# Kernel optimization log

Hardware: AMD Instinct MI355X
Metric: run time of the kernel (lower is better)

Reference implementation:

```python
import jax, jax.numpy as jnp
import numpy as np

B, N, D = 4, 2048, 256
H = 8
HD = D // H
FF = 1024
EPS = 1e-5


def layer_norm(x, g, b):
    mu = jnp.mean(x, axis=-1, keepdims=True)
    var = jnp.mean((x - mu) ** 2, axis=-1, keepdims=True)
    return (x - mu) * jax.lax.rsqrt(var + EPS) * g + b


def setup_inputs() -> dict:
    key = jax.random.key(0)
    ks = jax.random.split(key, 12)
    s = 0.02
    return {
        "tokens": jax.random.normal(ks[0], (B, N, D), dtype=jnp.float32),
        "key_padding_mask": jnp.zeros((B, N), dtype=bool),
        "ln1_g": jnp.ones((D,), jnp.float32),
        "ln1_b": jnp.zeros((D,), jnp.float32),
        "wq": jax.random.normal(ks[1], (D, D), jnp.float32) * s,
        "bq": jnp.zeros((D,), jnp.float32),
        "wk": jax.random.normal(ks[2], (D, D), jnp.float32) * s,
        "bk": jnp.zeros((D,), jnp.float32),
        "wv": jax.random.normal(ks[3], (D, D), jnp.float32) * s,
        "bv": jnp.zeros((D,), jnp.float32),
        "wo": jax.random.normal(ks[4], (D, D), jnp.float32) * s,
        "bo": jnp.zeros((D,), jnp.float32),
        "ln2_g": jnp.ones((D,), jnp.float32),
        "ln2_b": jnp.zeros((D,), jnp.float32),
        "w1": jax.random.normal(ks[5], (D, FF), jnp.float32) * s,
        "b1": jnp.zeros((FF,), jnp.float32),
        "w2": jax.random.normal(ks[6], (FF, D), jnp.float32) * s,
        "b2": jnp.zeros((D,), jnp.float32),
    }


def reference(tokens, key_padding_mask, ln1_g, ln1_b, wq, bq, wk, bk, wv, bv,
              wo, bo, ln2_g, ln2_b, w1, b1, w2, b2):
    x = tokens
    # --- self-attention sublayer (pre-LN) ---
    xn = layer_norm(x, ln1_g, ln1_b)
    q = (xn @ wq + bq).reshape(B, N, H, HD).transpose(0, 2, 1, 3)  # [B,H,N,HD]
    k = (xn @ wk + bk).reshape(B, N, H, HD).transpose(0, 2, 1, 3)
    v = (xn @ wv + bv).reshape(B, N, H, HD).transpose(0, 2, 1, 3)
    scores = jnp.einsum('bhqd,bhkd->bhqk', q, k) / np.sqrt(HD).astype(np.float32)
    scores = jnp.where(key_padding_mask[:, None, None, :], -jnp.inf, scores)
    probs = jax.nn.softmax(scores, axis=-1)
    attn = jnp.einsum('bhqk,bhkd->bhqd', probs, v)
    attn = attn.transpose(0, 2, 1, 3).reshape(B, N, D)
    x = x + (attn @ wo + bo)
    # --- feed-forward sublayer (pre-LN) ---
    xn2 = layer_norm(x, ln2_g, ln2_b)
    h = jax.nn.gelu(xn2 @ w1 + b1, approximate=False)  # torch GELU is exact erf
    x = x + (h @ w2 + b2)
    return x
```

## Files before the change

kernel.cpp:

```cpp
#include <hip/hip_runtime.h>
#include <cmath>

typedef __attribute__((ext_vector_type(8))) __bf16 bf16x8;
typedef __attribute__((ext_vector_type(4))) __bf16 bf16x4;
typedef __attribute__((ext_vector_type(4))) float  f32x4;

constexpr int NB   = 4;
constexpr int SEQ  = 2048;
constexpr int DM   = 256;
constexpr int NH   = 8;
constexpr int DH   = 32;
constexpr int DFF  = 1024;
constexpr int MTOK = NB * SEQ;

__global__ __launch_bounds__(256) void ln_kernel(const float* __restrict__ x,
                                                 const float* __restrict__ g,
                                                 const float* __restrict__ b,
                                                 __bf16* __restrict__ out) {
  int wave = threadIdx.x >> 6, lane = threadIdx.x & 63;
  int row = blockIdx.x * 4 + wave;
  const float* xr = x + (size_t)row * DM;
  f32x4 v = *(const f32x4*)(xr + lane * 4);
  float s  = v[0] + v[1] + v[2] + v[3];
  float sq = v[0]*v[0] + v[1]*v[1] + v[2]*v[2] + v[3]*v[3];
  #pragma unroll
  for (int off = 1; off < 64; off <<= 1) {
    s  += __shfl_xor(s, off);
    sq += __shfl_xor(sq, off);
  }
  float mu  = s * (1.0f / DM);
  float var = sq * (1.0f / DM) - mu * mu;
  float rs  = rsqrtf(var + 1e-5f);
  f32x4 gv = *(const f32x4*)(g + lane * 4);
  f32x4 bv = *(const f32x4*)(b + lane * 4);
  bf16x4 o;
  #pragma unroll
  for (int i = 0; i < 4; ++i) o[i] = (__bf16)((v[i] - mu) * rs * gv[i] + bv[i]);
  *(bf16x4*)(out + (size_t)row * DM + lane * 4) = o;
}

__global__ __launch_bounds__(256) void prep_kernel(
    const float* __restrict__ wq, const float* __restrict__ wk, const float* __restrict__ wv,
    const float* __restrict__ wo, const float* __restrict__ w1, const float* __restrict__ w2,
    const unsigned char* __restrict__ mask, const float* __restrict__ tokens,
    const float* __restrict__ ln1g, const float* __restrict__ ln1b,
    __bf16* __restrict__ wqkvT, __bf16* __restrict__ woT,
    __bf16* __restrict__ w1T, __bf16* __restrict__ w2T,
    float* __restrict__ madd_g, __bf16* __restrict__ xn1) {
  __shared__ float tile[32][33];
  int z = blockIdx.z;
  int tid = threadIdx.x;
  if (z == 6) {
    if (blockIdx.x) return;
    int idx = blockIdx.y * 256 + tid;
    madd_g[idx] = mask[idx] ? -__builtin_inff() : 0.0f;
    return;
  }
  if (z >= 7) {
    int lb = blockIdx.y * 32 + blockIdx.x;
    int row = (z - 7) * 4096 + lb * 4 + (tid >> 6);
    int lane = tid & 63;
    const float* xr = tokens + (size_t)row * DM;
    f32x4 v = *(const f32x4*)(xr + lane * 4);
    float s  = v[0] + v[1] + v[2] + v[3];
    float sq = v[0]*v[0] + v[1]*v[1] + v[2]*v[2] + v[3]*v[3];
    #pragma unroll
    for (int off = 1; off < 64; off <<= 1) {
      s  += __shfl_xor(s, off);
      sq += __shfl_xor(sq, off);
    }
    float mu  = s * (1.0f / DM);
    float var = sq * (1.0f / DM) - mu * mu;
    float rs  = rsqrtf(var + 1e-5f);
    f32x4 gv = *(const f32x4*)(ln1g + lane * 4);
    f32x4 bv = *(const f32x4*)(ln1b + lane * 4);
    bf16x4 o;
    #pragma unroll
    for (int i = 0; i < 4; ++i) o[i] = (__bf16)((v[i] - mu) * rs * gv[i] + bv[i]);
    *(bf16x4*)(xn1 + (size_t)row * DM + lane * 4) = o;
    return;
  }
  const float* W; __bf16* Wt; int K, N;
  if      (z == 0) { W = wq; Wt = wqkvT;          K = 256;  N = 256;  }
  else if (z == 1) { W = wk; Wt = wqkvT + 65536;  K = 256;  N = 256;  }
  else if (z == 2) { W = wv; Wt = wqkvT + 131072; K = 256;  N = 256;  }
  else if (z == 3) { W = wo; Wt = woT;            K = 256;  N = 256;  }
  else if (z == 4) { W = w1; Wt = w1T;            K = 256;  N = 1024; }
  else             { W = w2; Wt = w2T;            K = 1024; N = 256;  }
  int n0 = blockIdx.x * 32, k0 = blockIdx.y * 32;
  if (n0 >= N || k0 >= K) return;
  {
    int kl = tid >> 3, n4 = (tid & 7) * 4;
    f32x4 v = *(const f32x4*)(W + (size_t)(k0 + kl) * N + n0 + n4);
    tile[kl][n4 + 0] = v[0]; tile[kl][n4 + 1] = v[1];
    tile[kl][n4 + 2] = v[2]; tile[kl][n4 + 3] = v[3];
  }
  __syncthreads();
  {
    int nl = tid >> 3, k4 = (tid & 7) * 4;
    bf16x4 o;
    #pragma unroll
    for (int i = 0; i < 4; ++i) o[i] = (__bf16)tile[k4 + i][nl];
    *(bf16x4*)(Wt + (size_t)(n0 + nl) * K + k0 + k4) = o;
  }
}

__global__ __launch_bounds__(256) void transpose_v(const __bf16* __restrict__ V,
                                                   __bf16* __restrict__ Vt) {
  __shared__ __bf16 tile[64][40];
  int tok0 = blockIdx.x * 64;
  int bh = blockIdx.y;
  int tid = threadIdx.x;
  {
    int tl = tid >> 2, h8 = (tid & 3) * 8;
    *(bf16x8*)&tile[tl][h8] = *(const bf16x8*)(V + ((size_t)bh * SEQ + tok0 + tl) * DH + h8);
  }
  __syncthreads();
  {
    int hl = tid >> 3, t8 = (tid & 7) * 8;
    bf16x8 o;
    #pragma unroll
    for (int i = 0; i < 8; ++i) o[i] = tile[t8 + i][hl];
    *(bf16x8*)(Vt + ((size_t)bh * DH + hl) * SEQ + tok0 + t8) = o;
  }
}

template<int BM, int BN, int EP>
__global__ __launch_bounds__(256) void gemm_bt(
    const __bf16* __restrict__ A, const __bf16* __restrict__ Bt,
    int M, int N, int K,
    const float* __restrict__ bias,
    const float* __restrict__ bq, const float* __restrict__ bk, const float* __restrict__ bv,
    const float* __restrict__ resid, float* __restrict__ outf,
    __bf16* __restrict__ outb,
    __bf16* __restrict__ outq, __bf16* __restrict__ outk, __bf16* __restrict__ outv) {
  constexpr int MT = BM / 32, NT = BN / 32;
  constexpr int AP = BM / 32, BP = BN / 32;
  __shared__ __bf16 As[BM * 64];
  __shared__ __bf16 Bs[BN * 64];
  int tid = threadIdx.x;
  int wave = tid >> 6, lane = tid & 63;
  int wm = wave >> 1, wn = wave & 1;
  int quad = lane >> 4, l16 = lane & 15;
  int m0 = blockIdx.x * BM, n0 = blockIdx.y * BN;
  int lrow = lane >> 3;
  int lcg  = ((lane & 7) ^ lrow) * 8;

  f32x4 acc[MT][NT];
  #pragma unroll
  for (int mt = 0; mt < MT; ++mt)
    #pragma unroll
    for (int nt = 0; nt < NT; ++nt)
      #pragma unroll
      for (int r = 0; r < 4; ++r) acc[mt][nt][r] = 0.0f;

  bf16x8 ap[AP], bp[BP];
  #pragma unroll
  for (int i = 0; i < AP; ++i) {
    int rbase = wave * (BM / 4) + i * 8;
    ap[i] = *(const bf16x8*)(A + (size_t)(m0 + rbase + lrow) * K + lcg);
  }
  #pragma unroll
  for (int i = 0; i < BP; ++i) {
    int rbase = wave * (BN / 4) + i * 8;
    bp[i] = *(const bf16x8*)(Bt + (size_t)(n0 + rbase + lrow) * K + lcg);
  }
  #pragma unroll
  for (int i = 0; i < AP; ++i) {
    int rbase = wave * (BM / 4) + i * 8;
    *(bf16x8*)&As[rbase * 64 + lane * 8] = ap[i];
  }
  #pragma unroll
  for (int i = 0; i < BP; ++i) {
    int rbase = wave * (BN / 4) + i * 8;
    *(bf16x8*)&Bs[rbase * 64 + lane * 8] = bp[i];
  }
  __syncthreads();

  for (int kt = 0; kt < K; kt += 64) {
    bool more = (kt + 64) < K;
    if (more) {
      #pragma unroll
      for (int i = 0; i < AP; ++i) {
        int rbase = wave * (BM / 4) + i * 8;
        ap[i] = *(const bf16x8*)(A + (size_t)(m0 + rbase + lrow) * K + kt + 64 + lcg);
      }
      #pragma unroll
      for (int i = 0; i < BP; ++i) {
        int rbase = wave * (BN / 4) + i * 8;
        bp[i] = *(const bf16x8*)(Bt + (size_t)(n0 + rbase + lrow) * K + kt + 64 + lcg);
      }
    }
    #pragma unroll
    for (int ks = 0; ks < 2; ++ks) {
      bf16x8 af[MT], bfr[NT];
      #pragma unroll
      for (int mt = 0; mt < MT; ++mt) {
        int row = wm * (BM / 2) + mt * 16 + l16;
        af[mt] = *(const bf16x8*)&As[row * 64 + (((ks * 4 + quad) ^ (l16 & 7)) * 8)];
      }
      #pragma unroll
      for (int nt = 0; nt < NT; ++nt) {
        int row = wn * (BN / 2) + nt * 16 + l16;
        bfr[nt] = *(const bf16x8*)&Bs[row * 64 + (((ks * 4 + quad) ^ (l16 & 7)) * 8)];
      }
      #pragma unroll
      for (int mt = 0; mt < MT; ++mt)
        #pragma unroll
        for (int nt = 0; nt < NT; ++nt)
          acc[mt][nt] = __builtin_amdgcn_mfma_f32_16x16x32_bf16(af[mt], bfr[nt], acc[mt][nt], 0, 0, 0);
    }
    if (more) {
      __syncthreads();
      #pragma unroll
      for (int i = 0; i < AP; ++i) {
        int rbase = wave * (BM / 4) + i * 8;
        *(bf16x8*)&As[rbase * 64 + lane * 8] = ap[i];
      }
      #pragma unroll
      for (int i = 0; i < BP; ++i) {
        int rbase = wave * (BN / 4) + i * 8;
        *(bf16x8*)&Bs[rbase * 64 + lane * 8] = bp[i];
      }
      __syncthreads();
    }
  }

  #pragma unroll
  for (int mt = 0; mt < MT; ++mt)
  #pragma unroll
  for (int nt = 0; nt < NT; ++nt)
  #pragma unroll
  for (int r = 0; r < 4; ++r) {
    int gm = m0 + wm * (BM / 2) + mt * 16 + quad * 4 + r;
    int gn = n0 + wn * (BN / 2) + nt * 16 + l16;
    float v = acc[mt][nt][r];
    if constexpr (EP == 0) {
      int which = gn >> 8, nn = gn & 255;
      const float* bp2 = which == 0 ? bq : (which == 1 ? bk : bv);
      v += bp2[nn];
      int h = nn >> 5, hd = nn & 31;
      int bb = gm >> 11, tok = gm & 2047;
      __bf16* dst = which == 0 ? outq : (which == 1 ? outk : outv);
      dst[(((size_t)(bb * NH + h)) * SEQ + tok) * DH + hd] = (__bf16)v;
    } else if constexpr (EP == 1) {
      v += bias[gn] + resid[(size_t)gm * N + gn];
      outf[(size_t)gm * N + gn] = v;
    } else {
      v += bias[gn];
      outb[(size_t)gm * N + gn] = (__bf16)(0.5f * v * (1.0f + erff(v * 0.70710678118654752f)));
    }
  }
}

__global__ __launch_bounds__(64) void attn_kernel(
    const __bf16* __restrict__ Q, const __bf16* __restrict__ K,
    const __bf16* __restrict__ Vt, const float* __restrict__ madd_g,
    __bf16* __restrict__ out) {
  constexpr float C2 = 0.2550350030061664f;
  __shared__ __bf16 Ps[2][16][72];
  int bh = blockIdx.x;
  int qw = blockIdx.y * 32;
  int b  = bh >> 3, h = bh & 7;
  int lane = threadIdx.x & 63;
  int quad = lane >> 4, l16 = lane & 15;
  const __bf16* Qb = Q  + (size_t)bh * SEQ * DH;
  const __bf16* Kb = K  + (size_t)bh * SEQ * DH;
  const __bf16* Vb = Vt + (size_t)bh * DH * SEQ;
  const float* maddb = madd_g + b * SEQ;

  bf16x8 qf[2];
  #pragma unroll
  for (int qg = 0; qg < 2; ++qg)
    qf[qg] = *(const bf16x8*)(Qb + (size_t)(qw + qg * 16 + l16) * DH + quad * 8);

  bf16x8 ones;
  #pragma unroll
  for (int i = 0; i < 8; ++i) ones[i] = (__bf16)1.0f;

  f32x4 o[2][2], ol[2];
  #pragma unroll
  for (int qg = 0; qg < 2; ++qg) {
    #pragma unroll
    for (int nt = 0; nt < 2; ++nt)
      #pragma unroll
      for (int r = 0; r < 4; ++r) o[qg][nt][r] = 0.0f;
    #pragma unroll
    for (int r = 0; r < 4; ++r) ol[qg][r] = 0.0f;
  }

  for (int kt = 0; kt < SEQ / 64; ++kt) {
    int k0 = kt * 64;

    f32x4 s[2][4];
    f32x4 zf; zf[0] = zf[1] = zf[2] = zf[3] = 0.0f;
    #pragma unroll
    for (int mt = 0; mt < 4; ++mt) {
      bf16x8 kf = *(const bf16x8*)(Kb + (size_t)(k0 + mt * 16 + l16) * DH + quad * 8);
      s[0][mt] = __builtin_amdgcn_mfma_f32_16x16x32_bf16(kf, qf[0], zf, 0, 0, 0);
      s[1][mt] = __builtin_amdgcn_mfma_f32_16x16x32_bf16(kf, qf[1], zf, 0, 0, 0);
    }

    #pragma unroll
    for (int mt = 0; mt < 4; ++mt) {
      f32x4 md = *(const f32x4*)(maddb + k0 + mt * 16 + quad * 4);
      #pragma unroll
      for (int qg = 0; qg < 2; ++qg) {
        bf16x4 pv;
        #pragma unroll
        for (int r = 0; r < 4; ++r)
          pv[r] = (__bf16)__builtin_amdgcn_exp2f(fmaf(s[qg][mt][r], C2, md[r]));
        *(bf16x4*)&Ps[qg][l16][mt * 16 + quad * 4] = pv;
      }
    }

    #pragma unroll
    for (int ks = 0; ks < 2; ++ks) {
      bf16x8 vf[2];
      #pragma unroll
      for (int nt = 0; nt < 2; ++nt)
        vf[nt] = *(const bf16x8*)(Vb + (size_t)(nt * 16 + l16) * SEQ + k0 + ks * 32 + quad * 8);
      #pragma unroll
      for (int qg = 0; qg < 2; ++qg) {
        bf16x8 pf = *(const bf16x8*)&Ps[qg][l16][ks * 32 + quad * 8];
        #pragma unroll
        for (int nt = 0; nt < 2; ++nt)
          o[qg][nt] = __builtin_amdgcn_mfma_f32_16x16x32_bf16(pf, vf[nt], o[qg][nt], 0, 0, 0);
        ol[qg] = __builtin_amdgcn_mfma_f32_16x16x32_bf16(pf, ones, ol[qg], 0, 0, 0);
      }
    }
  }

  #pragma unroll
  for (int qg = 0; qg < 2; ++qg) {
    f32x4 inv;
    #pragma unroll
    for (int r = 0; r < 4; ++r) inv[r] = 1.0f / ol[qg][r];
    #pragma unroll
    for (int nt = 0; nt < 2; ++nt)
      #pragma unroll
      for (int r = 0; r < 4; ++r) {
        int q   = qw + qg * 16 + quad * 4 + r;
        int col = h * DH + nt * 16 + l16;
        out[((size_t)(b * SEQ + q)) * DM + col] = (__bf16)(o[qg][nt][r] * inv[r]);
      }
  }
}

extern "C" void kernel_launch(void* const* d_in, const int* in_sizes, int n_in,
                              void* d_out, int out_size, void* d_ws, size_t ws_size,
                              hipStream_t stream) {
  const float* tokens = (const float*)d_in[0];
  const unsigned char* mask = (const unsigned char*)d_in[1];
  const float* ln1g = (const float*)d_in[2];
  const float* ln1b = (const float*)d_in[3];
  const float* wq = (const float*)d_in[4];
  const float* bq = (const float*)d_in[5];
  const float* wk = (const float*)d_in[6];
  const float* bk = (const float*)d_in[7];
  const float* wv = (const float*)d_in[8];
  const float* bv = (const float*)d_in[9];
  const float* wo = (const float*)d_in[10];
  const float* bo = (const float*)d_in[11];
  const float* ln2g = (const float*)d_in[12];
  const float* ln2b = (const float*)d_in[13];
  const float* w1 = (const float*)d_in[14];
  const float* b1 = (const float*)d_in[15];
  const float* w2 = (const float*)d_in[16];
  const float* b2 = (const float*)d_in[17];
  float* out = (float*)d_out;
  char* ws = (char*)d_ws;

  __bf16* wqkvT = (__bf16*)(ws + 0);
  __bf16* woT   = (__bf16*)(ws + 393216);
  __bf16* w1T   = (__bf16*)(ws + 524288);
  __bf16* w2T   = (__bf16*)(ws + 1048576);
  __bf16* xn1   = (__bf16*)(ws + 1572864);
  __bf16* qb    = (__bf16*)(ws + 5767168);
  __bf16* kb    = (__bf16*)(ws + 9961472);
  __bf16* vb    = (__bf16*)(ws + 14155776);
  __bf16* vt    = (__bf16*)(ws + 18350080);
  __bf16* attn  = (__bf16*)(ws + 22544384);
  float*  x1    = (float*)(ws + 26738688);
  __bf16* xn2   = (__bf16*)(ws + 35127296);
  __bf16* hbuf  = (__bf16*)(ws + 39321600);
  float*  madd  = (float*)(ws + 56098816);

  prep_kernel<<<dim3(32, 32, 9), 256, 0, stream>>>(
      wq, wk, wv, wo, w1, w2, mask, tokens, ln1g, ln1b,
      wqkvT, woT, w1T, w2T, madd, xn1);

  gemm_bt<128, 128, 0><<<dim3(64, 6), 256, 0, stream>>>(
      xn1, wqkvT, MTOK, 768, 256, nullptr, bq, bk, bv,
      nullptr, nullptr, nullptr, qb, kb, vb);

  transpose_v<<<dim3(SEQ / 64, 32), 256, 0, stream>>>(vb, vt);

  attn_kernel<<<dim3(32, SEQ / 32), 64, 0, stream>>>(qb, kb, vt, madd, attn);

  gemm_bt<64, 64, 1><<<dim3(128, 4), 256, 0, stream>>>(
      attn, woT, MTOK, 256, 256, bo, nullptr, nullptr, nullptr,
      tokens, x1, nullptr, nullptr, nullptr, nullptr);

  ln_kernel<<<MTOK / 4, 256, 0, stream>>>(x1, ln2g, ln2b, xn2);

  gemm_bt<128, 128, 2><<<dim3(64, 8), 256, 0, stream>>>(
      xn2, w1T, MTOK, DFF, 256, b1, nullptr, nullptr, nullptr,
      nullptr, nullptr, hbuf, nullptr, nullptr, nullptr);

  gemm_bt<64, 64, 1><<<dim3(128, 4), 256, 0, stream>>>(
      hbuf, w2T, MTOK, 256, DFF, b2, nullptr, nullptr, nullptr,
      x1, out, nullptr, nullptr, nullptr, nullptr);
}
```

Baseline: 207.4 us.

## Compact prep grid, fuse V transpose into QKV epilogue, pipeline attention, fast GELU

The prep kernel now runs on a flat 1D grid with no empty blocks, where the old 3D grid of 32x32x9 launched many blocks that exited immediately. The QKV GEMM epilogue writes V straight into the transposed layout, so the separate transpose kernel and its extra pass over memory go away. The attention loop is software-pipelined with double-buffered P tiles: it computes the next tile's scores and exponentials while running the current PV MFMAs. GELU is replaced by a tanh-style sigmoid approximation built on exp2, which is cheaper than erff but changes the numerics slightly.

Result: no change. 209.2 us (+0.9%).

```diff
diff --git a/kernel.cpp b/kernel.cpp
--- a/kernel.cpp
+++ b/kernel.cpp
@@ -48,17 +48,10 @@
     __bf16* __restrict__ w1T, __bf16* __restrict__ w2T,
     float* __restrict__ madd_g, __bf16* __restrict__ xn1) {
   __shared__ float tile[32][33];
-  int z = blockIdx.z;
+  int bid = blockIdx.x;
   int tid = threadIdx.x;
-  if (z == 6) {
-    if (blockIdx.x) return;
-    int idx = blockIdx.y * 256 + tid;
-    madd_g[idx] = mask[idx] ? -__builtin_inff() : 0.0f;
-    return;
-  }
-  if (z >= 7) {
-    int lb = blockIdx.y * 32 + blockIdx.x;
-    int row = (z - 7) * 4096 + lb * 4 + (tid >> 6);
+  if (bid >= 800) {
+    int row = (bid - 800) * 4 + (tid >> 6);
     int lane = tid & 63;
     const float* xr = tokens + (size_t)row * DM;
     f32x4 v = *(const f32x4*)(xr + lane * 4);
@@ -80,15 +73,29 @@
     *(bf16x4*)(xn1 + (size_t)row * DM + lane * 4) = o;
     return;
   }
-  const float* W; __bf16* Wt; int K, N;
-  if      (z == 0) { W = wq; Wt = wqkvT;          K = 256;  N = 256;  }
-  else if (z == 1) { W = wk; Wt = wqkvT + 65536;  K = 256;  N = 256;  }
-  else if (z == 2) { W = wv; Wt = wqkvT + 131072; K = 256;  N = 256;  }
-  else if (z == 3) { W = wo; Wt = woT;            K = 256;  N = 256;  }
-  else if (z == 4) { W = w1; Wt = w1T;            K = 256;  N = 1024; }
-  else             { W = w2; Wt = w2T;            K = 1024; N = 256;  }
-  int n0 = blockIdx.x * 32, k0 = blockIdx.y * 32;
-  if (n0 >= N || k0 >= K) return;
+  if (bid >= 768) {
+    int idx = (bid - 768) * 256 + tid;
+    madd_g[idx] = mask[idx] ? -__builtin_inff() : 0.0f;
+    return;
+  }
+  const float* W; __bf16* Wt; int K, N, n0, k0;
+  if (bid < 256) {
+    int z = bid >> 6, local = bid & 63;
+    K = 256; N = 256;
+    n0 = (local & 7) * 32; k0 = (local >> 3) * 32;
+    if      (z == 0) { W = wq; Wt = wqkvT;          }
+    else if (z == 1) { W = wk; Wt = wqkvT + 65536;  }
+    else if (z == 2) { W = wv; Wt = wqkvT + 131072; }
+    else             { W = wo; Wt = woT;            }
+  } else if (bid < 512) {
+    int local = bid - 256;
+    W = w1; Wt = w1T; K = 256; N = 1024;
+    n0 = (local & 31) * 32; k0 = (local >> 5) * 32;
+  } else {
+    int local = bid - 512;
+    W = w2; Wt = w2T; K = 1024; N = 256;
+    n0 = (local & 7) * 32; k0 = (local >> 3) * 32;
+  }
   {
     int kl = tid >> 3, n4 = (tid & 7) * 4;
     f32x4 v = *(const f32x4*)(W + (size_t)(k0 + kl) * N + n0 + n4);
@@ -102,26 +109,6 @@
     #pragma unroll
     for (int i = 0; i < 4; ++i) o[i] = (__bf16)tile[k4 + i][nl];
     *(bf16x4*)(Wt + (size_t)(n0 + nl) * K + k0 + k4) = o;
-  }
-}
-
-__global__ __launch_bounds__(256) void transpose_v(const __bf16* __restrict__ V,
-                                                   __bf16* __restrict__ Vt) {
-  __shared__ __bf16 tile[64][40];
-  int tok0 = blockIdx.x * 64;
-  int bh = blockIdx.y;
-  int tid = threadIdx.x;
-  {
-    int tl = tid >> 2, h8 = (tid & 3) * 8;
-    *(bf16x8*)&tile[tl][h8] = *(const bf16x8*)(V + ((size_t)bh * SEQ + tok0 + tl) * DH + h8);
-  }
-  __syncthreads();
-  {
-    int hl = tid >> 3, t8 = (tid & 7) * 8;
-    bf16x8 o;
-    #pragma unroll
-    for (int i = 0; i < 8; ++i) o[i] = tile[t8 + i][hl];
-    *(bf16x8*)(Vt + ((size_t)bh * DH + hl) * SEQ + tok0 + t8) = o;
   }
 }
 
@@ -241,14 +228,20 @@
       v += bp2[nn];
       int h = nn >> 5, hd = nn & 31;
       int bb = gm >> 11, tok = gm & 2047;
-      __bf16* dst = which == 0 ? outq : (which == 1 ? outk : outv);
-      dst[(((size_t)(bb * NH + h)) * SEQ + tok) * DH + hd] = (__bf16)v;
+      if (which == 2) {
+        outv[(((size_t)(bb * NH + h)) * DH + hd) * SEQ + tok] = (__bf16)v;
+      } else {
+        __bf16* dst = which == 0 ? outq : outk;
+        dst[(((size_t)(bb * NH + h)) * SEQ + tok) * DH + hd] = (__bf16)v;
+      }
     } else if constexpr (EP == 1) {
       v += bias[gn] + resid[(size_t)gm * N + gn];
       outf[(size_t)gm * N + gn] = v;
     } else {
       v += bias[gn];
-      outb[(size_t)gm * N + gn] = (__bf16)(0.5f * v * (1.0f + erff(v * 0.70710678118654752f)));
+      float v2 = v * v;
+      float t = __builtin_amdgcn_exp2f(v * (2.3022082f + 0.10294324f * v2));
+      outb[(size_t)gm * N + gn] = (__bf16)(v * t * __builtin_amdgcn_rcpf(t + 1.0f));
     }
   }
 }
@@ -258,7 +251,8 @@
     const __bf16* __restrict__ Vt, const float* __restrict__ madd_g,
     __bf16* __restrict__ out) {
   constexpr float C2 = 0.2550350030061664f;
-  __shared__ __bf16 Ps[2][16][72];
+  constexpr int NT = SEQ / 64;
+  __shared__ __bf16 Ps[2][2][16][72];
   int bh = blockIdx.x;
   int qw = blockIdx.y * 32;
   int b  = bh >> 3, h = bh & 7;
@@ -289,46 +283,85 @@
     for (int r = 0; r < 4; ++r) ol[qg][r] = 0.0f;
   }
 
-  for (int kt = 0; kt < SEQ / 64; ++kt) {
-    int k0 = kt * 64;
-
+  f32x4 zf; zf[0] = zf[1] = zf[2] = zf[3] = 0.0f;
+
+  {
     f32x4 s[2][4];
-    f32x4 zf; zf[0] = zf[1] = zf[2] = zf[3] = 0.0f;
     #pragma unroll
     for (int mt = 0; mt < 4; ++mt) {
-      bf16x8 kf = *(const bf16x8*)(Kb + (size_t)(k0 + mt * 16 + l16) * DH + quad * 8);
+      bf16x8 kf = *(const bf16x8*)(Kb + (size_t)(mt * 16 + l16) * DH + quad * 8);
       s[0][mt] = __builtin_amdgcn_mfma_f32_16x16x32_bf16(kf, qf[0], zf, 0, 0, 0);
       s[1][mt] = __builtin_amdgcn_mfma_f32_16x16x32_bf16(kf, qf[1], zf, 0, 0, 0);
     }
-
     #pragma unroll
     for (int mt = 0; mt < 4; ++mt) {
-      f32x4 md = *(const f32x4*)(maddb + k0 + mt * 16 + quad * 4);
+      f32x4 md = *(const f32x4*)(maddb + mt * 16 + quad * 4);
       #pragma unroll
       for (int qg = 0; qg < 2; ++qg) {
         bf16x4 pv;
         #pragma unroll
         for (int r = 0; r < 4; ++r)
           pv[r] = (__bf16)__builtin_amdgcn_exp2f(fmaf(s[qg][mt][r], C2, md[r]));
-        *(bf16x4*)&Ps[qg][l16][mt * 16 + quad * 4] = pv;
-      }
-    }
-
-    #pragma unroll
-    for (int ks = 0; ks < 2; ++ks) {
-      bf16x8 vf[2];
+        *(bf16x4*)&Ps[0][qg][l16][mt * 16 + quad * 4] = pv;
+      }
+    }
+  }
+
+  int buf = 0;
+  for (int kt = 0; kt < NT; ++kt) {
+    int k0 = kt * 64;
+    bool more = (kt + 1) < NT;
+
+    bf16x8 kf[4];
+    if (more) {
+      #pragma unroll
+      for (int mt = 0; mt < 4; ++mt)
+        kf[mt] = *(const bf16x8*)(Kb + (size_t)(k0 + 64 + mt * 16 + l16) * DH + quad * 8);
+    }
+    bf16x8 vf[2][2];
+    #pragma unroll
+    for (int ks = 0; ks < 2; ++ks)
       #pragma unroll
       for (int nt = 0; nt < 2; ++nt)
-        vf[nt] = *(const bf16x8*)(Vb + (size_t)(nt * 16 + l16) * SEQ + k0 + ks * 32 + quad * 8);
+        vf[ks][nt] = *(const bf16x8*)(Vb + (size_t)(nt * 16 + l16) * SEQ + k0 + ks * 32 + quad * 8);
+    bf16x8 pf[2][2];
+    #pragma unroll
+    for (int ks = 0; ks < 2; ++ks)
+      #pragma unroll
+      for (int qg = 0; qg < 2; ++qg)
+        pf[ks][qg] = *(const bf16x8*)&Ps[buf][qg][l16][ks * 32 + quad * 8];
+
+    #pragma unroll
+    for (int ks = 0; ks < 2; ++ks)
       #pragma unroll
       for (int qg = 0; qg < 2; ++qg) {
-        bf16x8 pf = *(const bf16x8*)&Ps[qg][l16][ks * 32 + quad * 8];
         #pragma unroll
         for (int nt = 0; nt < 2; ++nt)
-          o[qg][nt] = __builtin_amdgcn_mfma_f32_16x16x32_bf16(pf, vf[nt], o[qg][nt], 0, 0, 0);
-        ol[qg] = __builtin_amdgcn_mfma_f32_16x16x32_bf16(pf, ones, ol[qg], 0, 0, 0);
-      }
-    }
+          o[qg][nt] = __builtin_amdgcn_mfma_f32_16x16x32_bf16(pf[ks][qg], vf[ks][nt], o[qg][nt], 0, 0, 0);
+        ol[qg] = __builtin_amdgcn_mfma_f32_16x16x32_bf16(pf[ks][qg], ones, ol[qg], 0, 0, 0);
+      }
+
+    if (more) {
+      f32x4 s[2][4];
+      #pragma unroll
+      for (int mt = 0; mt < 4; ++mt) {
+        s[0][mt] = __builtin_amdgcn_mfma_f32_16x16x32_bf16(kf[mt], qf[0], zf, 0, 0, 0);
+        s[1][mt] = __builtin_amdgcn_mfma_f32_16x16x32_bf16(kf[mt], qf[1], zf, 0, 0, 0);
+      }
+      #pragma unroll
+      for (int mt = 0; mt < 4; ++mt) {
+        f32x4 md = *(const f32x4*)(maddb + k0 + 64 + mt * 16 + quad * 4);
+        #pragma unroll
+        for (int qg = 0; qg < 2; ++qg) {
+          bf16x4 pv;
+          #pragma unroll
+          for (int r = 0; r < 4; ++r)
+            pv[r] = (__bf16)__builtin_amdgcn_exp2f(fmaf(s[qg][mt][r], C2, md[r]));
+          *(bf16x4*)&Ps[buf ^ 1][qg][l16][mt * 16 + quad * 4] = pv;
+        }
+      }
+    }
+    buf ^= 1;
   }
 
   #pragma unroll
@@ -378,7 +411,6 @@
   __bf16* xn1   = (__bf16*)(ws + 1572864);
   __bf16* qb    = (__bf16*)(ws + 5767168);
   __bf16* kb    = (__bf16*)(ws + 9961472);
-  __bf16* vb    = (__bf16*)(ws + 14155776);
   __bf16* vt    = (__bf16*)(ws + 18350080);
   __bf16* attn  = (__bf16*)(ws + 22544384);
   float*  x1    = (float*)(ws + 26738688);
@@ -386,15 +418,13 @@
   __bf16* hbuf  = (__bf16*)(ws + 39321600);
   float*  madd  = (float*)(ws + 56098816);
 
-  prep_kernel<<<dim3(32, 32, 9), 256, 0, stream>>>(
+  prep_kernel<<<2848, 256, 0, stream>>>(
       wq, wk, wv, wo, w1, w2, mask, tokens, ln1g, ln1b,
       wqkvT, woT, w1T, w2T, madd, xn1);
 
   gemm_bt<128, 128, 0><<<dim3(64, 6), 256, 0, stream>>>(
       xn1, wqkvT, MTOK, 768, 256, nullptr, bq, bk, bv,
-      nullptr, nullptr, nullptr, qb, kb, vb);
-
-  transpose_v<<<dim3(SEQ / 64, 32), 256, 0, stream>>>(vb, vt);
+      nullptr, nullptr, nullptr, qb, kb, vt);
 
   attn_kernel<<<dim3(32, SEQ / 32), 64, 0, stream>>>(qb, kb, vt, madd, attn);
 
```
